# Kernel tuning notes

Measured on AMD Instinct MI355X. Metric: run time of the kernel, lower is better.

The kernel has to match this reference:

```python
import jax, jax.numpy as jnp
import numpy as np

EPS = 1e-08

def _householder(x, v):
    # x: [B,S,r], v: [B,S,r]; H x = x - 2 v_n (v_n . x), v_n = v/||v||
    v_norm_sq = jnp.sum(v * v, axis=-1, keepdims=True) + EPS
    v_n = v / jnp.sqrt(v_norm_sq)
    vTx = jnp.sum(x * v_n, axis=-1, keepdims=True)
    return x - 2.0 * v_n * vTx

def setup_inputs() -> dict:
    key = jax.random.key(0)
    ks = jax.random.split(key, 8)
    B, S, D, R = 4, 4096, 1024, 256
    N_IN, N_PROC, N_OUT, K = 16, 64, 16, 8
    x = jax.random.normal(ks[0], (B, S, D), dtype=jnp.float32)
    input_idx = jax.random.randint(ks[1], (B, S), 0, N_IN)
    process_indices = jax.random.randint(ks[2], (B, S, K), 0, N_PROC)
    output_idx = jax.random.randint(ks[3], (B, S), 0, N_OUT)
    # learned params (orthogonal-ish init approximated by scaled gaussian)
    input_neurons = jax.random.normal(ks[4], (N_IN, D, R), dtype=jnp.float32) / np.sqrt(D)
    pv = jax.random.normal(ks[5], (N_PROC, R), dtype=jnp.float32)
    process_neurons = pv / (jnp.linalg.norm(pv, axis=-1, keepdims=True) + EPS)
    output_neurons = jax.random.normal(ks[6], (N_OUT, R, D), dtype=jnp.float32) / np.sqrt(D)
    return {"x": x, "input_neurons": input_neurons, "process_neurons": process_neurons,
            "output_neurons": output_neurons, "input_idx": input_idx,
            "process_indices": process_indices, "output_idx": output_idx}

def reference(x, input_neurons, process_neurons, output_neurons,
              input_idx, process_indices, output_idx):
    # ---- input projection (hard selection): d_model -> rank ----
    # compute all-expert projections then gather per token (avoids [B,S,D,R] gather)
    all_in = jnp.einsum('bsd,ndr->bsnr', x, input_neurons)          # [B,S,n_in,R]
    h = jnp.take_along_axis(all_in, input_idx[..., None, None], axis=2)[:, :, 0, :]  # [B,S,R]
    # ---- process: k sequential Householder reflections ----
    selected_v = process_neurons[process_indices]                    # [B,S,k,R]
    vs = jnp.moveaxis(selected_v, 2, 0)                              # [k,B,S,R]
    def step(carry, v):
        return _householder(carry, v), None
    h, _ = jax.lax.scan(step, h, vs)
    # ---- output projection (hard selection): rank -> d_model ----
    all_out = jnp.einsum('bsr,nrd->bsnd', h, output_neurons)         # [B,S,n_out,D]
    out = jnp.take_along_axis(all_out, output_idx[..., None, None], axis=2)[:, :, 0, :]
    return out
```

## Files before the change

kernel.cpp:

```cpp
#include <hip/hip_runtime.h>
#include <hip/hip_bf16.h>

#define NT    16384
#define DM    1024
#define RK    256
#define N_IN  16
#define N_OUT 16
#define KHH   8
#define MAXTOK 1536
#define BM    64
#define TPE   (MAXTOK / BM)
#define KC    4
#define GEMM_BLKS (8 * TPE * 16)
#define TWOUT_BLKS (16 * 64)
#define CVT_BLKS  2048

typedef short bf16x8 __attribute__((ext_vector_type(8)));
typedef float f32x4 __attribute__((ext_vector_type(4)));
typedef unsigned short u16;
typedef u16 u16x8 __attribute__((ext_vector_type(8)));
typedef u16 u16x4 __attribute__((ext_vector_type(4)));

__device__ __forceinline__ u16 f2bf(float f) {
  __hip_bfloat16 b = __float2bfloat16(f);
  return *reinterpret_cast<u16*>(&b);
}
__device__ __forceinline__ float bf2f(u16 u) {
  return __uint_as_float((unsigned)u << 16);
}

__device__ __forceinline__ void gl_lds16(const void* g, void* lds) {
  __builtin_amdgcn_global_load_lds(
      (const __attribute__((address_space(1))) void*)g,
      (__attribute__((address_space(3))) void*)lds, 16, 0, 0);
}

__device__ __forceinline__ void transpose_tile(
    const float* __restrict__ src, u16* __restrict__ dst,
    int R, int C, int e, int tile, float (*ls)[65], int t) {
  const int tilesC = C >> 6;
  const int tr = (tile / tilesC) << 6;
  const int tc = (tile % tilesC) << 6;
  const int row = t >> 2, q = t & 3;
  const float* s = src + (size_t)e * R * C + (size_t)(tr + row) * C + tc + q * 16;
#pragma unroll
  for (int j = 0; j < 4; j++) {
    const float4 v = ((const float4*)s)[j];
    ls[row][q * 16 + j * 4 + 0] = v.x;
    ls[row][q * 16 + j * 4 + 1] = v.y;
    ls[row][q * 16 + j * 4 + 2] = v.z;
    ls[row][q * 16 + j * 4 + 3] = v.w;
  }
  __syncthreads();
  const int cc = t >> 2;
  u16x8 o0, o1;
#pragma unroll
  for (int j = 0; j < 8; j++) o0[j] = f2bf(ls[q * 16 + j][cc]);
#pragma unroll
  for (int j = 0; j < 8; j++) o1[j] = f2bf(ls[q * 16 + 8 + j][cc]);
  u16* d = dst + (size_t)e * C * R + (size_t)(tc + cc) * R + tr + q * 16;
  ((u16x8*)d)[0] = o0;
  ((u16x8*)d)[1] = o1;
}

__global__ __launch_bounds__(256) void lists_pn_winT_cvt(
    const int* __restrict__ in_idx, const int* __restrict__ out_idx,
    const float* __restrict__ pn, const float* __restrict__ Win,
    const float* __restrict__ x,
    int* __restrict__ list_in, int* __restrict__ cnt_in,
    int* __restrict__ list_out, int* __restrict__ cnt_out,
    float* __restrict__ pnorm2, u16* __restrict__ WinT,
    u16* __restrict__ xb) {
  const int b = blockIdx.x;
  const int tid = threadIdx.x, lane = tid & 63, wid = tid >> 6;
  __shared__ float ls[64][65];
  __shared__ int wsum[4];

  if (b >= 33 + 1024) {
    const int bc = b - (33 + 1024);
#pragma unroll
    for (int g = 0; g < 4; ++g) {
      const size_t i = (size_t)bc * 256 + tid + (size_t)g * (CVT_BLKS * 256);
      const float4 a = ((const float4*)x)[2 * i];
      const float4 c = ((const float4*)x)[2 * i + 1];
      u16x8 o;
      o[0] = f2bf(a.x); o[1] = f2bf(a.y); o[2] = f2bf(a.z); o[3] = f2bf(a.w);
      o[4] = f2bf(c.x); o[5] = f2bf(c.y); o[6] = f2bf(c.z); o[7] = f2bf(c.w);
      ((u16x8*)xb)[i] = o;
    }
    return;
  }
  if (b >= 33) {
    const int b2 = b - 33;
    const int e = b2 >> 6, tile = b2 & 63;
    const int tilesC = RK >> 6;
    const int tr = (tile / tilesC) << 6;
    const int tc = (tile % tilesC) << 6;
    const int row = tid >> 2, q = tid & 3;
    const float* s = Win + (size_t)e * DM * RK + (size_t)(tr + row) * RK + tc + q * 16;
#pragma unroll
    for (int j = 0; j < 4; j++) {
      const float4 v = ((const float4*)s)[j];
      ls[row][q * 16 + j * 4 + 0] = v.x;
      ls[row][q * 16 + j * 4 + 1] = v.y;
      ls[row][q * 16 + j * 4 + 2] = v.z;
      ls[row][q * 16 + j * 4 + 3] = v.w;
    }
    __syncthreads();
    const int cc = tid >> 2;
    u16x8 o0, o1;
#pragma unroll
    for (int j = 0; j < 8; j++) o0[j] = f2bf(ls[q * 16 + j][cc]);
#pragma unroll
    for (int j = 0; j < 8; j++) o1[j] = f2bf(ls[q * 16 + 8 + j][cc]);
    const int D = tr + q * 16;
    const int kc = D >> 8, dk = D & 255;
    u16* d = WinT + ((size_t)(e * KC + kc) * RK + (tc + cc)) * 256 + dk;
    ((u16x8*)d)[0] = o0;
    ((u16x8*)d)[1] = o1;
    return;
  }
  if (b == 32) {
    const int p = tid >> 2, q = tid & 3;
    const float* row = pn + (size_t)p * RK + q * 64;
    float s = 0.f;
#pragma unroll
    for (int i = 0; i < 16; i++) {
      const float4 v = ((const float4*)row)[i];
      s += v.x * v.x + v.y * v.y + v.z * v.z + v.w * v.w;
    }
    s += __shfl_xor(s, 1);
    s += __shfl_xor(s, 2);
    if (q == 0) pnorm2[p] = s + 1e-8f;
    return;
  }

  const int e = b & 15, which = b >> 4;
  const int* __restrict__ idx = which ? out_idx : in_idx;
  int* __restrict__ list = (which ? list_out : list_in) + (size_t)e * NT;
  int* __restrict__ cnt = (which ? cnt_out : cnt_in) + e;

  const unsigned long long lt = (1ull << lane) - 1ull;
  int off = 0;
  for (int base = 0; base < NT; base += 1024) {
    const int4 iv = ((const int4*)(idx + base))[tid];
    const bool f0 = iv.x == e, f1 = iv.y == e, f2 = iv.z == e, f3 = iv.w == e;
    const unsigned long long m0 = __ballot(f0), m1 = __ballot(f1),
                             m2 = __ballot(f2), m3 = __ballot(f3);
    const int below = __popcll(m0 & lt) + __popcll(m1 & lt) +
                      __popcll(m2 & lt) + __popcll(m3 & lt);
    const int wtot = __popcll(m0) + __popcll(m1) + __popcll(m2) + __popcll(m3);
    if (lane == 0) wsum[wid] = wtot;
    __syncthreads();
    int b0 = 0, tot = 0;
#pragma unroll
    for (int w = 0; w < 4; w++) { if (w < wid) b0 += wsum[w]; tot += wsum[w]; }
    int pos = off + b0 + below;
    const int t = base + tid * 4;
    if (f0) list[pos++] = t;
    if (f1) list[pos++] = t + 1;
    if (f2) list[pos++] = t + 2;
    if (f3) list[pos++] = t + 3;
    off += tot;
    __syncthreads();
  }
  if (tid == 0) *cnt = off;
}

__global__ __launch_bounds__(256, 6) void input_gemm_woT(
    const u16* __restrict__ xb, const u16* __restrict__ WinT,
    const int* __restrict__ list, const int* __restrict__ cnt,
    u16* __restrict__ h4,
    const float* __restrict__ Wout, u16* __restrict__ WoT) {
  __shared__ __align__(16) char smem[24832];
  const int tid = threadIdx.x, lane = tid & 63, w = tid >> 6;
  const int bid = blockIdx.x;

  if (bid >= GEMM_BLKS) {
    const int b2 = bid - GEMM_BLKS;
    transpose_tile(Wout, WoT, RK, DM, b2 >> 6, b2 & 63,
                   (float(*)[65])smem, tid);
    return;
  }

  const int xcd = bid & 7;
  int j = bid >> 3;
  const int tile = j % TPE;
  j /= TPE;
  const int nb = j & 1;
  const int e = xcd * 2 + ((j >> 1) & 1);
  const int kc = j >> 2;
  const int nt = cnt[e];
  const int t0 = tile * BM;
  if (t0 >= nt) return;
  const int* __restrict__ lst = list + (size_t)e * NT + t0;
  const int ntok = min(BM, nt - t0);

  u16* As = (u16*)smem;
  u16* Bs = (u16*)(smem + 8192);
  int* toks = (int*)(smem + 8192 + 16384);

  if (tid < BM) toks[tid] = lst[tid < ntok ? tid : 0];
  __syncthreads();

  const int sub = lane >> 3;
  const int swz8 = ((lane & 7) ^ sub) * 8;
  const u16* Wbase = WinT + ((size_t)(e * KC + kc) * RK + nb * 128) * 256;
  const int ar0 = (w * 2 + 0) * 8 + sub;
  const int ar1 = (w * 2 + 1) * 8 + sub;
  const u16* asrc0 = xb + (size_t)toks[ar0] * DM + kc * 256 + swz8;
  const u16* asrc1 = xb + (size_t)toks[ar1] * DM + kc * 256 + swz8;

  f32x4 acc[4][2];
#pragma unroll
  for (int m = 0; m < 4; m++)
#pragma unroll
    for (int jx = 0; jx < 2; jx++) acc[m][jx] = (f32x4)0.f;

  const int l15 = lane & 15, lg = lane >> 4;

#pragma unroll
  for (int it = 0; it < 4; ++it) {
    const int k0 = it * 64;
    if (it) __syncthreads();
    gl_lds16(asrc0 + k0, As + (w * 2 + 0) * 512);
    gl_lds16(asrc1 + k0, As + (w * 2 + 1) * 512);
#pragma unroll
    for (int i = 0; i < 4; ++i) {
      const int g = w * 4 + i;
      const int n = g * 8 + sub;
      gl_lds16(Wbase + (size_t)n * 256 + k0 + swz8, Bs + g * 512);
    }
    __syncthreads();
#pragma unroll
    for (int kk = 0; kk < 2; ++kk) {
      const int sw = (((kk * 4 + lg) ^ (l15 & 7)) << 4);
      bf16x8 fa[4];
#pragma unroll
      for (int m = 0; m < 4; ++m)
        fa[m] = *(const bf16x8*)((const char*)As + (m * 16 + l15) * 128 + sw);
#pragma unroll
      for (int jx = 0; jx < 2; ++jx) {
        const int n = w * 32 + jx * 16 + l15;
        const bf16x8 fb = *(const bf16x8*)((const char*)Bs + n * 128 + sw);
#pragma unroll
        for (int m = 0; m < 4; ++m)
          acc[m][jx] = __builtin_amdgcn_mfma_f32_16x16x32_bf16(fa[m], fb, acc[m][jx], 0, 0, 0);
      }
    }
  }

  u16* hp4 = h4 + (size_t)kc * NT * RK;
#pragma unroll
  for (int m = 0; m < 4; ++m)
#pragma unroll
    for (int r = 0; r < 4; ++r) {
      const int slot = m * 16 + lg * 4 + r;
      if (slot < ntok) {
        u16* hp = hp4 + (size_t)toks[slot] * RK + nb * 128 + w * 32 + l15;
#pragma unroll
        for (int jx = 0; jx < 2; ++jx) hp[jx * 16] = f2bf(acc[m][jx][r]);
      }
    }
}

__global__ __launch_bounds__(256) void hh_k(
    const u16* __restrict__ h4, u16* __restrict__ hb,
    const float* __restrict__ pn, const float* __restrict__ pnorm2,
    const int* __restrict__ pidx) {
  const int lane = threadIdx.x & 63;
  const int t = blockIdx.x * 4 + (threadIdx.x >> 6);

  float4 hv;
  {
    const u16x4 p0 = ((const u16x4*)(h4 + ((size_t)0 * NT + t) * RK))[lane];
    const u16x4 p1 = ((const u16x4*)(h4 + ((size_t)1 * NT + t) * RK))[lane];
    const u16x4 p2 = ((const u16x4*)(h4 + ((size_t)2 * NT + t) * RK))[lane];
    const u16x4 p3 = ((const u16x4*)(h4 + ((size_t)3 * NT + t) * RK))[lane];
    hv.x = (bf2f(p0[0]) + bf2f(p1[0])) + (bf2f(p2[0]) + bf2f(p3[0]));
    hv.y = (bf2f(p0[1]) + bf2f(p1[1])) + (bf2f(p2[1]) + bf2f(p3[1]));
    hv.z = (bf2f(p0[2]) + bf2f(p1[2])) + (bf2f(p2[2]) + bf2f(p3[2]));
    hv.w = (bf2f(p0[3]) + bf2f(p1[3])) + (bf2f(p2[3]) + bf2f(p3[3]));
  }

#pragma unroll
  for (int k = 0; k < KHH; k++) {
    const int p = pidx[t * KHH + k];
    const float4 v = ((const float4*)(pn + (size_t)p * RK))[lane];
    float dvh = v.x * hv.x + v.y * hv.y + v.z * hv.z + v.w * hv.w;
#pragma unroll
    for (int s = 32; s; s >>= 1) dvh += __shfl_xor(dvh, s);
    const float c = 2.f * dvh / pnorm2[p];
    hv.x = fmaf(-c, v.x, hv.x);
    hv.y = fmaf(-c, v.y, hv.y);
    hv.z = fmaf(-c, v.z, hv.z);
    hv.w = fmaf(-c, v.w, hv.w);
  }
  u16x4 o;
  o[0] = f2bf(hv.x); o[1] = f2bf(hv.y); o[2] = f2bf(hv.z); o[3] = f2bf(hv.w);
  ((u16x4*)(hb + (size_t)t * RK))[lane] = o;
}

__global__ __launch_bounds__(256, 6) void output_gemm_mfma(
    const u16* __restrict__ hb, const u16* __restrict__ WoT,
    const int* __restrict__ list, const int* __restrict__ cnt,
    float* __restrict__ out) {
  const int bid = blockIdx.x;
  const int xcd = bid & 7;
  int j = bid >> 3;
  const int tile = j % TPE;
  j /= TPE;
  const int e = xcd * 2 + (j & 1);
  const int cb = j >> 1;
  const int nt = cnt[e];
  const int t0 = tile * BM;
  if (t0 >= nt) return;
  const int* __restrict__ lst = list + (size_t)e * NT + t0;
  const int ntok = min(BM, nt - t0);

  __shared__ __align__(16) u16 As[BM * 64];
  __shared__ __align__(16) u16 Bs[128 * 64];
  __shared__ int toks[BM];

  const int tid = threadIdx.x, lane = tid & 63, w = tid >> 6;
  if (tid < BM) toks[tid] = lst[tid < ntok ? tid : 0];
  __syncthreads();

  const int sub = lane >> 3;
  const int swz8 = ((lane & 7) ^ sub) * 8;
  const u16* Wbase = WoT + (size_t)e * DM * RK + (size_t)(cb * 128) * RK;
  const int ar0 = (w * 2 + 0) * 8 + sub;
  const int ar1 = (w * 2 + 1) * 8 + sub;
  const u16* asrc0 = hb + (size_t)toks[ar0] * RK + swz8;
  const u16* asrc1 = hb + (size_t)toks[ar1] * RK + swz8;

  f32x4 acc[4][2];
#pragma unroll
  for (int m = 0; m < 4; m++)
#pragma unroll
    for (int jx = 0; jx < 2; jx++) acc[m][jx] = (f32x4)0.f;

  const int l15 = lane & 15, lg = lane >> 4;

#pragma unroll
  for (int it = 0; it < RK / 64; ++it) {
    const int k0 = it * 64;
    if (it) __syncthreads();
    gl_lds16(asrc0 + k0, As + (w * 2 + 0) * 512);
    gl_lds16(asrc1 + k0, As + (w * 2 + 1) * 512);
#pragma unroll
    for (int i = 0; i < 4; ++i) {
      const int g = w * 4 + i;
      const int n = g * 8 + sub;
      gl_lds16(Wbase + (size_t)n * RK + k0 + swz8, Bs + g * 512);
    }
    __syncthreads();
#pragma unroll
    for (int kk = 0; kk < 2; ++kk) {
      const int sw = (((kk * 4 + lg) ^ (l15 & 7)) << 4);
      bf16x8 fa[4];
#pragma unroll
      for (int m = 0; m < 4; ++m)
        fa[m] = *(const bf16x8*)((const char*)As + (m * 16 + l15) * 128 + sw);
#pragma unroll
      for (int jx = 0; jx < 2; ++jx) {
        const int n = w * 32 + jx * 16 + l15;
        const bf16x8 fb = *(const bf16x8*)((const char*)Bs + n * 128 + sw);
#pragma unroll
        for (int m = 0; m < 4; ++m)
          acc[m][jx] = __builtin_amdgcn_mfma_f32_16x16x32_bf16(fa[m], fb, acc[m][jx], 0, 0, 0);
      }
    }
  }

#pragma unroll
  for (int m = 0; m < 4; ++m)
#pragma unroll
    for (int r = 0; r < 4; ++r) {
      const int slot = m * 16 + lg * 4 + r;
      if (slot < ntok) {
        float* op = out + (size_t)toks[slot] * DM + cb * 128 + w * 32 + l15;
#pragma unroll
        for (int jx = 0; jx < 2; ++jx) op[jx * 16] = acc[m][jx][r];
      }
    }
}

extern "C" void kernel_launch(void* const* d_in, const int* in_sizes, int n_in,
                              void* d_out, int out_size, void* d_ws,
                              size_t ws_size, hipStream_t stream) {
  const float* x     = (const float*)d_in[0];
  const float* Win   = (const float*)d_in[1];
  const float* pn    = (const float*)d_in[2];
  const float* Wout  = (const float*)d_in[3];
  const int* in_idx  = (const int*)d_in[4];
  const int* pidx    = (const int*)d_in[5];
  const int* out_idx = (const int*)d_in[6];
  float* out = (float*)d_out;

  char* ws = (char*)d_ws;
  u16* WinT  = (u16*)ws;                    ws += (size_t)N_IN * RK * DM * 2;
  u16* WoT   = (u16*)ws;                    ws += (size_t)N_OUT * DM * RK * 2;
  u16* hb    = (u16*)ws;                    ws += (size_t)NT * RK * 2;
  u16* h4    = (u16*)ws;                    ws += (size_t)KC * NT * RK * 2;
  u16* xb    = (u16*)ws;                    ws += (size_t)NT * DM * 2;
  int* list_in  = (int*)ws;                 ws += (size_t)N_IN * NT * 4;
  int* list_out = (int*)ws;                 ws += (size_t)N_OUT * NT * 4;
  int* cnt_in   = (int*)ws;                 ws += 64;
  int* cnt_out  = (int*)ws;                 ws += 64;
  float* pnorm2 = (float*)ws;

  hipLaunchKernelGGL(lists_pn_winT_cvt, dim3(33 + 1024 + CVT_BLKS), dim3(256),
                     0, stream, in_idx, out_idx, pn, Win, x, list_in, cnt_in,
                     list_out, cnt_out, pnorm2, WinT, xb);
  hipLaunchKernelGGL(input_gemm_woT, dim3(GEMM_BLKS + TWOUT_BLKS), dim3(256),
                     0, stream, xb, WinT, list_in, cnt_in, h4, Wout, WoT);
  hipLaunchKernelGGL(hh_k, dim3(NT / 4), dim3(256), 0, stream,
                     h4, hb, pn, pnorm2, pidx);
  hipLaunchKernelGGL(output_gemm_mfma, dim3(GEMM_BLKS), dim3(256), 0, stream,
                     hb, WoT, list_out, cnt_out, out);
}
```

Before: 85.27 us.

## Pre-gather tokens into expert-contiguous bf16 buffer and store GEMM output compactly

New measurement: 107.9 us. +26.6%, slower.

```diff
diff --git a/kernel.cpp b/kernel.cpp
--- a/kernel.cpp
+++ b/kernel.cpp
@@ -7,13 +7,13 @@
 #define N_IN  16
 #define N_OUT 16
 #define KHH   8
-#define MAXTOK 1536
+#define MAXTOK 1280
 #define BM    64
 #define TPE   (MAXTOK / BM)
 #define KC    4
-#define GEMM_BLKS (8 * TPE * 16)
+#define IN_BLKS  (8 * TPE * 16)
+#define OUT_BLKS (8 * TPE * 16)
 #define TWOUT_BLKS (16 * 64)
-#define CVT_BLKS  2048
 
 typedef short bf16x8 __attribute__((ext_vector_type(8)));
 typedef float f32x4 __attribute__((ext_vector_type(4)));
@@ -63,33 +63,17 @@
   ((u16x8*)d)[1] = o1;
 }
 
-__global__ __launch_bounds__(256) void lists_pn_winT_cvt(
+__global__ __launch_bounds__(256) void lists_pn_winT(
     const int* __restrict__ in_idx, const int* __restrict__ out_idx,
     const float* __restrict__ pn, const float* __restrict__ Win,
-    const float* __restrict__ x,
     int* __restrict__ list_in, int* __restrict__ cnt_in,
     int* __restrict__ list_out, int* __restrict__ cnt_out,
-    float* __restrict__ pnorm2, u16* __restrict__ WinT,
-    u16* __restrict__ xb) {
+    float* __restrict__ pnorm2, u16* __restrict__ WinT) {
   const int b = blockIdx.x;
   const int tid = threadIdx.x, lane = tid & 63, wid = tid >> 6;
   __shared__ float ls[64][65];
   __shared__ int wsum[4];
 
-  if (b >= 33 + 1024) {
-    const int bc = b - (33 + 1024);
-#pragma unroll
-    for (int g = 0; g < 4; ++g) {
-      const size_t i = (size_t)bc * 256 + tid + (size_t)g * (CVT_BLKS * 256);
-      const float4 a = ((const float4*)x)[2 * i];
-      const float4 c = ((const float4*)x)[2 * i + 1];
-      u16x8 o;
-      o[0] = f2bf(a.x); o[1] = f2bf(a.y); o[2] = f2bf(a.z); o[3] = f2bf(a.w);
-      o[4] = f2bf(c.x); o[5] = f2bf(c.y); o[6] = f2bf(c.z); o[7] = f2bf(c.w);
-      ((u16x8*)xb)[i] = o;
-    }
-    return;
-  }
   if (b >= 33) {
     const int b2 = b - 33;
     const int e = b2 >> 6, tile = b2 & 63;
@@ -167,17 +151,42 @@
   if (tid == 0) *cnt = off;
 }
 
+__global__ __launch_bounds__(256) void gather_cvt(
+    const float* __restrict__ x, const int* __restrict__ list_in,
+    const int* __restrict__ cnt_in, u16* __restrict__ xg) {
+  const int bid = blockIdx.x;
+  const int e = bid / (MAXTOK / 16);
+  const int sg = bid % (MAXTOK / 16);
+  const int tid = threadIdx.x;
+  const int row = tid >> 4;
+  const int slot = sg * 16 + row;
+  if (slot >= cnt_in[e]) return;
+  const int tok = list_in[(size_t)e * NT + slot];
+  const int c0 = (tid & 15) * 64;
+  const int kc = c0 >> 8, dk = c0 & 255;
+  const float* xp = x + (size_t)tok * DM + c0;
+  u16* dst = xg + ((size_t)(e * KC + kc) * MAXTOK + slot) * 256 + dk;
+#pragma unroll
+  for (int i = 0; i < 8; ++i) {
+    const float4 a = ((const float4*)xp)[2 * i];
+    const float4 c = ((const float4*)xp)[2 * i + 1];
+    u16x8 o;
+    o[0] = f2bf(a.x); o[1] = f2bf(a.y); o[2] = f2bf(a.z); o[3] = f2bf(a.w);
+    o[4] = f2bf(c.x); o[5] = f2bf(c.y); o[6] = f2bf(c.z); o[7] = f2bf(c.w);
+    ((u16x8*)dst)[i] = o;
+  }
+}
+
 __global__ __launch_bounds__(256, 6) void input_gemm_woT(
-    const u16* __restrict__ xb, const u16* __restrict__ WinT,
-    const int* __restrict__ list, const int* __restrict__ cnt,
-    u16* __restrict__ h4,
+    const u16* __restrict__ xg, const u16* __restrict__ WinT,
+    const int* __restrict__ cnt_in, u16* __restrict__ h4,
     const float* __restrict__ Wout, u16* __restrict__ WoT) {
   __shared__ __align__(16) char smem[24832];
   const int tid = threadIdx.x, lane = tid & 63, w = tid >> 6;
   const int bid = blockIdx.x;
 
-  if (bid >= GEMM_BLKS) {
-    const int b2 = bid - GEMM_BLKS;
+  if (bid >= IN_BLKS) {
+    const int b2 = bid - IN_BLKS;
     transpose_tile(Wout, WoT, RK, DM, b2 >> 6, b2 & 63,
                    (float(*)[65])smem, tid);
     return;
@@ -187,29 +196,23 @@
   int j = bid >> 3;
   const int tile = j % TPE;
   j /= TPE;
-  const int nb = j & 1;
+  const int cb = j & 1;
   const int e = xcd * 2 + ((j >> 1) & 1);
   const int kc = j >> 2;
-  const int nt = cnt[e];
   const int t0 = tile * BM;
-  if (t0 >= nt) return;
-  const int* __restrict__ lst = list + (size_t)e * NT + t0;
-  const int ntok = min(BM, nt - t0);
+  if (t0 >= cnt_in[e]) return;
 
   u16* As = (u16*)smem;
   u16* Bs = (u16*)(smem + 8192);
-  int* toks = (int*)(smem + 8192 + 16384);
-
-  if (tid < BM) toks[tid] = lst[tid < ntok ? tid : 0];
-  __syncthreads();
 
   const int sub = lane >> 3;
   const int swz8 = ((lane & 7) ^ sub) * 8;
-  const u16* Wbase = WinT + ((size_t)(e * KC + kc) * RK + nb * 128) * 256;
+  const u16* Wbase = WinT + ((size_t)(e * KC + kc) * RK + cb * 128) * 256;
   const int ar0 = (w * 2 + 0) * 8 + sub;
   const int ar1 = (w * 2 + 1) * 8 + sub;
-  const u16* asrc0 = xb + (size_t)toks[ar0] * DM + kc * 256 + swz8;
-  const u16* asrc1 = xb + (size_t)toks[ar1] * DM + kc * 256 + swz8;
+  const u16* xgbase = xg + (size_t)(e * KC + kc) * MAXTOK * 256;
+  const u16* asrc0 = xgbase + (size_t)(t0 + ar0) * 256 + swz8;
+  const u16* asrc1 = xgbase + (size_t)(t0 + ar1) * 256 + swz8;
 
   f32x4 acc[4][2];
 #pragma unroll
@@ -250,33 +253,38 @@
     }
   }
 
-  u16* hp4 = h4 + (size_t)kc * NT * RK;
+  u16* hp4 = h4 + ((size_t)(kc * N_IN + e) * MAXTOK + t0) * 256 + cb * 128;
 #pragma unroll
   for (int m = 0; m < 4; ++m)
 #pragma unroll
     for (int r = 0; r < 4; ++r) {
       const int slot = m * 16 + lg * 4 + r;
-      if (slot < ntok) {
-        u16* hp = hp4 + (size_t)toks[slot] * RK + nb * 128 + w * 32 + l15;
-#pragma unroll
-        for (int jx = 0; jx < 2; ++jx) hp[jx * 16] = f2bf(acc[m][jx][r]);
-      }
+      u16* hp = hp4 + (size_t)slot * 256 + w * 32 + l15;
+#pragma unroll
+      for (int jx = 0; jx < 2; ++jx) hp[jx * 16] = f2bf(acc[m][jx][r]);
     }
 }
 
 __global__ __launch_bounds__(256) void hh_k(
     const u16* __restrict__ h4, u16* __restrict__ hb,
     const float* __restrict__ pn, const float* __restrict__ pnorm2,
-    const int* __restrict__ pidx) {
+    const int* __restrict__ pidx, const int* __restrict__ list_in,
+    const int* __restrict__ cnt_in) {
+  const int bid = blockIdx.x;
+  const int e = bid / (MAXTOK / 4);
+  const int sg = bid % (MAXTOK / 4);
   const int lane = threadIdx.x & 63;
-  const int t = blockIdx.x * 4 + (threadIdx.x >> 6);
+  const int slot = sg * 4 + (threadIdx.x >> 6);
+  if (slot >= cnt_in[e]) return;
+  const int t = list_in[(size_t)e * NT + slot];
 
   float4 hv;
   {
-    const u16x4 p0 = ((const u16x4*)(h4 + ((size_t)0 * NT + t) * RK))[lane];
-    const u16x4 p1 = ((const u16x4*)(h4 + ((size_t)1 * NT + t) * RK))[lane];
-    const u16x4 p2 = ((const u16x4*)(h4 + ((size_t)2 * NT + t) * RK))[lane];
-    const u16x4 p3 = ((const u16x4*)(h4 + ((size_t)3 * NT + t) * RK))[lane];
+    const size_t base = (size_t)e * MAXTOK + slot;
+    const u16x4 p0 = ((const u16x4*)(h4 + ((size_t)(0 * N_IN) * MAXTOK + base) * 256))[lane];
+    const u16x4 p1 = ((const u16x4*)(h4 + ((size_t)(1 * N_IN) * MAXTOK + base) * 256))[lane];
+    const u16x4 p2 = ((const u16x4*)(h4 + ((size_t)(2 * N_IN) * MAXTOK + base) * 256))[lane];
+    const u16x4 p3 = ((const u16x4*)(h4 + ((size_t)(3 * N_IN) * MAXTOK + base) * 256))[lane];
     hv.x = (bf2f(p0[0]) + bf2f(p1[0])) + (bf2f(p2[0]) + bf2f(p3[0]));
     hv.y = (bf2f(p0[1]) + bf2f(p1[1])) + (bf2f(p2[1]) + bf2f(p3[1]));
     hv.z = (bf2f(p0[2]) + bf2f(p1[2])) + (bf2f(p2[2]) + bf2f(p3[2]));
@@ -401,22 +409,24 @@
   char* ws = (char*)d_ws;
   u16* WinT  = (u16*)ws;                    ws += (size_t)N_IN * RK * DM * 2;
   u16* WoT   = (u16*)ws;                    ws += (size_t)N_OUT * DM * RK * 2;
+  u16* xg    = (u16*)ws;                    ws += (size_t)N_IN * KC * MAXTOK * 256 * 2;
+  u16* h4    = (u16*)ws;                    ws += (size_t)KC * N_IN * MAXTOK * 256 * 2;
   u16* hb    = (u16*)ws;                    ws += (size_t)NT * RK * 2;
-  u16* h4    = (u16*)ws;                    ws += (size_t)KC * NT * RK * 2;
-  u16* xb    = (u16*)ws;                    ws += (size_t)NT * DM * 2;
   int* list_in  = (int*)ws;                 ws += (size_t)N_IN * NT * 4;
   int* list_out = (int*)ws;                 ws += (size_t)N_OUT * NT * 4;
   int* cnt_in   = (int*)ws;                 ws += 64;
   int* cnt_out  = (int*)ws;                 ws += 64;
   float* pnorm2 = (float*)ws;
 
-  hipLaunchKernelGGL(lists_pn_winT_cvt, dim3(33 + 1024 + CVT_BLKS), dim3(256),
-                     0, stream, in_idx, out_idx, pn, Win, x, list_in, cnt_in,
-                     list_out, cnt_out, pnorm2, WinT, xb);
-  hipLaunchKernelGGL(input_gemm_woT, dim3(GEMM_BLKS + TWOUT_BLKS), dim3(256),
-                     0, stream, xb, WinT, list_in, cnt_in, h4, Wout, WoT);
-  hipLaunchKernelGGL(hh_k, dim3(NT / 4), dim3(256), 0, stream,
-                     h4, hb, pn, pnorm2, pidx);
-  hipLaunchKernelGGL(output_gemm_mfma, dim3(GEMM_BLKS), dim3(256), 0, stream,
+  hipLaunchKernelGGL(lists_pn_winT, dim3(33 + 1024), dim3(256), 0, stream,
+                     in_idx, out_idx, pn, Win, list_in, cnt_in,
+                     list_out, cnt_out, pnorm2, WinT);
+  hipLaunchKernelGGL(gather_cvt, dim3(N_IN * (MAXTOK / 16)), dim3(256), 0,
+                     stream, x, list_in, cnt_in, xg);
+  hipLaunchKernelGGL(input_gemm_woT, dim3(IN_BLKS + TWOUT_BLKS), dim3(256),
+                     0, stream, xg, WinT, cnt_in, h4, Wout, WoT);
+  hipLaunchKernelGGL(hh_k, dim3(N_IN * (MAXTOK / 4)), dim3(256), 0, stream,
+                     h4, hb, pn, pnorm2, pidx, list_in, cnt_in);
+  hipLaunchKernelGGL(output_gemm_mfma, dim3(OUT_BLKS), dim3(256), 0, stream,
                      hb, WoT, list_out, cnt_out, out);
 }
```
